# Optimization experiments

Hardware: AMD Instinct MI355X
Metric: run time of the kernel (lower is better)

The kernel has to match this reference:

```python
import jax, jax.numpy as jnp
import numpy as np

B, S, D_IN, D_OUT = 4, 4096, 256, 64


def setup_inputs() -> dict:
    key = jax.random.key(0)
    k1, k2, k3, k4, k5, k6 = jax.random.split(key, 6)
    return {
        "inputs_for_keys": jax.random.normal(k1, (B, S, D_IN), dtype=jnp.float32),
        "inputs_for_values": jax.random.normal(k2, (B, S, D_IN), dtype=jnp.float32),
        "inputs_for_queries": jax.random.normal(k3, (B, S, D_IN), dtype=jnp.float32),
        "wq": jax.random.normal(k4, (D_IN, D_OUT), dtype=jnp.float32) * 0.05,
        "wk": jax.random.normal(k5, (D_IN, D_OUT), dtype=jnp.float32) * 0.05,
        "wv": jax.random.normal(k6, (D_IN, D_OUT), dtype=jnp.float32) * 0.05,
    }


def reference(inputs_for_keys, inputs_for_values, inputs_for_queries, wq, wk, wv):
    # Linear projections: [B,S,D_IN] x [D_IN,D_OUT] -> [B,S,D_OUT]
    K = jnp.einsum("bsd,de->bse", inputs_for_keys, wk)
    V = jnp.einsum("bsd,de->bse", inputs_for_values, wv)
    Q = jnp.einsum("bsd,de->bse", inputs_for_queries, wq)
    d = K.shape[2]
    # Scaled dot-product scores: [B, S_q, S_k]
    scores = jnp.einsum("bqe,bke->bqk", Q, K) / jnp.sqrt(jnp.float32(d))
    # Causal mask: -inf where key index j > query index i (strict upper triangle)
    q_idx = jnp.arange(Q.shape[1])[:, None]
    k_idx = jnp.arange(K.shape[1])[None, :]
    mask = jnp.where(k_idx > q_idx, -jnp.inf, 0.0).astype(scores.dtype)
    scores = scores + mask[None, :, :]
    weights = jax.nn.softmax(scores, axis=-1)
    return jnp.einsum("bqk,bke->bqe", weights, V)
```

## Files before the change

kernel.cpp:

```cpp
#include <hip/hip_runtime.h>

#define S_LEN 4096
#define D_IN 256
#define D_OUT 64
#define BATCH 4
#define BQ 128
#define NQT (S_LEN / BQ)

typedef short bf16x8 __attribute__((ext_vector_type(8)));
typedef float f32x4 __attribute__((ext_vector_type(4)));

union L16 { int4 i; bf16x8 s; ushort u[8]; };
union U8  { uint2 d; ushort u[4]; };

#define SWZ(row, chunk) (((row) << 7) + ((((chunk) ^ ((row) & 7))) << 4))

#define QSCALE 0.1803368801111137f

__device__ inline ushort f2bf(float x) {
    unsigned u = __builtin_bit_cast(unsigned, x);
    u += 0x7FFFu + ((u >> 16) & 1u);
    return (ushort)(u >> 16);
}
__device__ inline ushort f2bf_t(float x) {
    return (ushort)(__builtin_bit_cast(unsigned, x) >> 16);
}
__device__ inline float bf2f(ushort h) {
    return __builtin_bit_cast(float, (unsigned)h << 16);
}

__global__ __launch_bounds__(256) void wsplit_kernel(
    const float* __restrict__ wq, const float* __restrict__ wk, const float* __restrict__ wv,
    ushort* __restrict__ Wt)
{
    const float* W = (blockIdx.y == 0) ? wq : (blockIdx.y == 1) ? wk : wv;
    __shared__ float Ws[64][68];
    const int t  = threadIdx.x;
    const int k0 = blockIdx.x * 64;
#pragma unroll
    for (int i = 0; i < 4; ++i) {
        int idx = t + i * 256;
        int r = idx >> 4, c4 = (idx & 15) * 4;
        *reinterpret_cast<float4*>(&Ws[r][c4]) =
            *reinterpret_cast<const float4*>(&W[(size_t)(k0 + r) * 64 + c4]);
    }
    __syncthreads();
    const int n = t >> 2, kc = t & 3;
    ushort h[16];
#pragma unroll
    for (int i = 0; i < 16; ++i) h[i] = f2bf(Ws[kc * 16 + i][n]);
    ushort* dst = Wt + ((size_t)blockIdx.y * 64 + n) * 256 + k0 + kc * 16;
    *reinterpret_cast<int4*>(dst)     = *reinterpret_cast<int4*>(h);
    *reinterpret_cast<int4*>(dst + 8) = *reinterpret_cast<int4*>(h + 8);
}

__global__ __launch_bounds__(256) void proj_kernel(
    const float* __restrict__ Xq, const float* __restrict__ Xk, const float* __restrict__ Xv,
    const ushort* __restrict__ Wt,
    ushort* __restrict__ Qb, ushort* __restrict__ Kb, ushort* __restrict__ Vtb)
{
    const float* X = (blockIdx.y == 0) ? Xq : (blockIdx.y == 1) ? Xk : Xv;
    const ushort* Wtp = Wt + (size_t)blockIdx.y * 64 * 256;

    __shared__ __align__(16) ushort Ob[64][64];

    const int t    = threadIdx.x;
    const int lane = t & 63;
    const int w    = t >> 6;
    const int n    = lane & 15;
    const int g    = lane >> 4;
    const int row0 = blockIdx.x * 64;

    const float* xrow = X + (size_t)(row0 + 16 * w + n) * D_IN;

    f32x4 acc[4];
    const f32x4 zero4 = {0.f, 0.f, 0.f, 0.f};
#pragma unroll
    for (int nt = 0; nt < 4; ++nt) acc[nt] = zero4;

#pragma unroll
    for (int kt = 0; kt < 8; ++kt) {
        const float4 c0 = *reinterpret_cast<const float4*>(xrow + kt * 32 + 8 * g);
        const float4 c1 = *reinterpret_cast<const float4*>(xrow + kt * 32 + 8 * g + 4);
        L16 wb[4];
#pragma unroll
        for (int nt = 0; nt < 4; ++nt)
            wb[nt].i = *reinterpret_cast<const int4*>(
                &Wtp[(size_t)(16 * nt + n) * 256 + kt * 32 + 8 * g]);

        const float xv[8] = {c0.x, c0.y, c0.z, c0.w, c1.x, c1.y, c1.z, c1.w};
        L16 xh, xl;
#pragma unroll
        for (int i = 0; i < 8; ++i) {
            ushort h = f2bf(xv[i]);
            xh.u[i] = h;
            xl.u[i] = f2bf(xv[i] - bf2f(h));
        }
#pragma unroll
        for (int nt = 0; nt < 4; ++nt) {
            acc[nt] = __builtin_amdgcn_mfma_f32_16x16x32_bf16(xh.s, wb[nt].s, acc[nt], 0, 0, 0);
            acc[nt] = __builtin_amdgcn_mfma_f32_16x16x32_bf16(xl.s, wb[nt].s, acc[nt], 0, 0, 0);
        }
    }

    const bool isV = (blockIdx.y == 2);
    const float oscale = (blockIdx.y == 0) ? QSCALE : 1.0f;
#pragma unroll
    for (int j = 0; j < 4; ++j) {
#pragma unroll
        for (int nt = 0; nt < 4; ++nt) {
            ushort h = f2bf(acc[nt][j] * oscale);
            int r = 16 * w + 4 * g + j;
            int c = 16 * nt + n;
            if (isV) Ob[c][r] = h; else Ob[r][c] = h;
        }
    }
    __syncthreads();
    const int b  = row0 >> 12;
    const int s0 = row0 & 4095;
#pragma unroll
    for (int i = 0; i < 2; ++i) {
        int idx = t + i * 256;
        int r = idx >> 3, c8 = (idx & 7) * 8;
        int4 v = *reinterpret_cast<const int4*>(&Ob[r][c8]);
        if (blockIdx.y == 0)
            *reinterpret_cast<int4*>(&Qb[(size_t)(row0 + r) * 64 + c8]) = v;
        else if (blockIdx.y == 1)
            *reinterpret_cast<int4*>(&Kb[(size_t)(row0 + r) * 64 + c8]) = v;
        else
            *reinterpret_cast<int4*>(&Vtb[((size_t)b * 64 + r) * S_LEN + s0 + c8]) = v;
    }
}

__global__ __launch_bounds__(256) void attn_kernel(
    const ushort* __restrict__ Q, const ushort* __restrict__ K,
    const ushort* __restrict__ Vt, float* __restrict__ O,
    ushort* __restrict__ Opart, float* __restrict__ Mpart, float* __restrict__ Lpart,
    int chunk_keys, int NCH, int lr4q, int Llive)
{
    __shared__ __align__(16) ushort Ks[2][64 * 64];
    __shared__ __align__(16) ushort Vs[2][64 * 64];
    __shared__ __align__(16) ushort Ps[4 * 16 * 64];

    const int Rq = 1 << lr4q;

    const int b = blockIdx.x & 3;
    const int f = blockIdx.x >> 2;
    int c = 0;
    while (NQT * (c + 1) - ((Rq * (c + 1) * c) >> 1) <= f) ++c;
    const int off  = NQT * c - ((Rq * c * (c - 1)) >> 1);
    const int qt   = (NQT - 1) - (f - off);
    const int ch   = c;
    const int q0   = qt * BQ;
    const int c0   = ch * chunk_keys;
    const int nchq = (qt >> lr4q) + 1;

    const int t    = threadIdx.x;
    const int lane = t & 63;
    const int w    = t >> 6;
    const int n    = lane & 15;
    const int g    = lane >> 4;

    const int kend = (c0 + chunk_keys < q0 + BQ) ? c0 + chunk_keys : q0 + BQ;
    const int kt0  = c0 >> 6;
    const int kt1  = (kend + 63) >> 6;

    const ushort* Qp = Q  + (size_t)b * S_LEN * 64;
    const ushort* Kp = K  + (size_t)b * S_LEN * 64;
    const ushort* Vp = Vt + (size_t)b * 64 * S_LEN;

    char* PsB = (char*)Ps + w * 2048;

    const int wqmin = q0 + 32 * w;
    const int wqmax = wqmin + 31;

    L16 aq[2][2];
#pragma unroll
    for (int h = 0; h < 2; ++h) {
        const size_t qr = (size_t)(wqmin + 16 * h + n) * 64;
        aq[h][0].i = *reinterpret_cast<const int4*>(&Qp[qr + 8 * g]);
        aq[h][1].i = *reinterpret_cast<const int4*>(&Qp[qr + 32 + 8 * g]);
    }

    L16 ones;
    ones.i = make_int4(0x3F803F80, 0x3F803F80, 0x3F803F80, 0x3F803F80);

    f32x4 oacc[2][4];
    const f32x4 zero4 = {0.f, 0.f, 0.f, 0.f};
#pragma unroll
    for (int h = 0; h < 2; ++h)
#pragma unroll
        for (int nt = 0; nt < 4; ++nt) oacc[h][nt] = zero4;
    float mreg[2] = {-1e30f, -1e30f}, lreg[2] = {0.f, 0.f};

    const int srow = t >> 3, sc = t & 7;

    auto load_tile = [&](int4 (&kr)[2], int4 (&vr)[2], int kt_) {
        const int kk0 = kt_ << 6;
#pragma unroll
        for (int i = 0; i < 2; ++i) {
            int row = srow + i * 32;
            kr[i] = *reinterpret_cast<const int4*>(&Kp[(size_t)(kk0 + row) * 64 + sc * 8]);
            vr[i] = *reinterpret_cast<const int4*>(&Vp[(size_t)row * S_LEN + kk0 + sc * 8]);
        }
    };
    auto store_tile = [&](int buf, const int4 (&kr)[2], const int4 (&vr)[2]) {
        char* kb = (char*)Ks + buf * 8192;
        char* vb = (char*)Vs + buf * 8192;
#pragma unroll
        for (int i = 0; i < 2; ++i) {
            int row = srow + i * 32;
            *reinterpret_cast<int4*>(kb + SWZ(row, sc)) = kr[i];
            *reinterpret_cast<int4*>(vb + SWZ(row, sc)) = vr[i];
        }
    };

    int4 kv[2], vv[2];
    load_tile(kv, vv, kt0);
    store_tile(0, kv, vv);
    if (kt0 + 1 < kt1) load_tile(kv, vv, kt0 + 1);
    __syncthreads();

    int cur = 0;
    for (int kt = kt0; kt < kt1; ++kt) {
        const int k0 = kt << 6;
        if (kt + 1 < kt1) {
            store_tile(cur ^ 1, kv, vv);
            if (kt + 2 < kt1) load_tile(kv, vv, kt + 2);
        }

        if (k0 <= wqmax) {
            char* KsB = (char*)Ks + cur * 8192;
            char* VsB = (char*)Vs + cur * 8192;

            f32x4 cS[2][4];
            __builtin_amdgcn_s_setprio(1);
#pragma unroll
            for (int t4 = 0; t4 < 4; ++t4) {
                L16 k0f, k1f;
                k0f.i = *reinterpret_cast<const int4*>(KsB + SWZ(16 * t4 + n, g));
                k1f.i = *reinterpret_cast<const int4*>(KsB + SWZ(16 * t4 + n, 4 + g));
#pragma unroll
                for (int h = 0; h < 2; ++h) {
                    f32x4 z = zero4;
                    z          = __builtin_amdgcn_mfma_f32_16x16x32_bf16(k0f.s, aq[h][0].s, z, 0, 0, 0);
                    cS[h][t4]  = __builtin_amdgcn_mfma_f32_16x16x32_bf16(k1f.s, aq[h][1].s, z, 0, 0, 0);
                }
            }
            __builtin_amdgcn_s_setprio(0);

#pragma unroll
            for (int h = 0; h < 2; ++h) {
                const int qrow = wqmin + 16 * h + n;
                float sc4[4][4];
#pragma unroll
                for (int t4 = 0; t4 < 4; ++t4)
#pragma unroll
                    for (int j = 0; j < 4; ++j) sc4[t4][j] = cS[h][t4][j];
                if (k0 + 63 > qrow) {
                    const int kb = k0 + 4 * g;
#pragma unroll
                    for (int t4 = 0; t4 < 4; ++t4)
#pragma unroll
                        for (int j = 0; j < 4; ++j)
                            if (kb + 16 * t4 + j > qrow) sc4[t4][j] = -1e30f;
                }

                float m0 = fmaxf(fmaxf(sc4[0][0], sc4[0][1]), fmaxf(sc4[0][2], sc4[0][3]));
                float m1 = fmaxf(fmaxf(sc4[1][0], sc4[1][1]), fmaxf(sc4[1][2], sc4[1][3]));
                float m2 = fmaxf(fmaxf(sc4[2][0], sc4[2][1]), fmaxf(sc4[2][2], sc4[2][3]));
                float m3 = fmaxf(fmaxf(sc4[3][0], sc4[3][1]), fmaxf(sc4[3][2], sc4[3][3]));
                const float lmax = fmaxf(fmaxf(m0, m1), fmaxf(m2, m3));

                if (__any(lmax > mreg[h] + 8.f)) {
                    float mx = lmax;
                    mx = fmaxf(mx, __shfl_xor(mx, 16, 64));
                    mx = fmaxf(mx, __shfl_xor(mx, 32, 64));
                    const float mnew  = fmaxf(mreg[h], mx);
                    const float alpha = exp2f(mreg[h] - mnew);
                    mreg[h] = mnew;
                    lreg[h] *= alpha;
#pragma unroll
                    for (int nt = 0; nt < 4; ++nt)
#pragma unroll
                        for (int j = 0; j < 4; ++j) oacc[h][nt][j] *= alpha;
                }

#pragma unroll
                for (int t4 = 0; t4 < 4; ++t4) {
                    U8 pw;
#pragma unroll
                    for (int j = 0; j < 4; ++j)
                        pw.u[j] = f2bf_t(exp2f(sc4[t4][j] - mreg[h]));
                    *reinterpret_cast<uint2*>(PsB + SWZ(n, 2 * t4 + (g >> 1)) + 8 * (g & 1)) = pw.d;
                }

                asm volatile("s_waitcnt lgkmcnt(0)" ::: "memory");
                L16 pa0, pa1;
                pa0.i = *reinterpret_cast<const int4*>(PsB + SWZ(n, g));
                pa1.i = *reinterpret_cast<const int4*>(PsB + SWZ(n, 4 + g));
                f32x4 ls = zero4;
                ls = __builtin_amdgcn_mfma_f32_16x16x32_bf16(ones.s, pa0.s, ls, 0, 0, 0);
                ls = __builtin_amdgcn_mfma_f32_16x16x32_bf16(ones.s, pa1.s, ls, 0, 0, 0);
                __builtin_amdgcn_s_setprio(1);
#pragma unroll
                for (int nt = 0; nt < 4; ++nt) {
                    L16 bv0, bv1;
                    bv0.i = *reinterpret_cast<const int4*>(VsB + SWZ(16 * nt + n, g));
                    bv1.i = *reinterpret_cast<const int4*>(VsB + SWZ(16 * nt + n, 4 + g));
                    oacc[h][nt] = __builtin_amdgcn_mfma_f32_16x16x32_bf16(bv0.s, pa0.s, oacc[h][nt], 0, 0, 0);
                    oacc[h][nt] = __builtin_amdgcn_mfma_f32_16x16x32_bf16(bv1.s, pa1.s, oacc[h][nt], 0, 0, 0);
                }
                __builtin_amdgcn_s_setprio(0);
                lreg[h] += ls[0];
            }
        }
        __syncthreads();
        cur ^= 1;
    }

    if (nchq == 1) {
#pragma unroll
        for (int h = 0; h < 2; ++h) {
            const float inv = 1.f / lreg[h];
            float* orow = O + ((size_t)b * S_LEN + wqmin + 16 * h + n) * 64;
#pragma unroll
            for (int nt = 0; nt < 4; ++nt)
#pragma unroll
                for (int j = 0; j < 4; ++j)
                    orow[16 * nt + 4 * g + j] = oacc[h][nt][j] * inv;
        }
    } else {
        const size_t slot = (size_t)((qt << 2) | b) * NCH + ch;
#pragma unroll
        for (int h = 0; h < 2; ++h) {
#pragma unroll
            for (int nt = 0; nt < 4; ++nt) {
                U8 pw;
#pragma unroll
                for (int j = 0; j < 4; ++j) pw.u[j] = f2bf(oacc[h][nt][j]);
                *reinterpret_cast<uint2*>(PsB + SWZ(n, 2 * nt + (g >> 1)) + 8 * (g & 1)) = pw.d;
            }
            asm volatile("s_waitcnt lgkmcnt(0)" ::: "memory");
            ushort* dst = Opart + slot * (BQ * 64) + w * 2048 + h * 1024;
#pragma unroll
            for (int i = 0; i < 2; ++i) {
                int ii = i * 64 + lane;
                *reinterpret_cast<int4*>(dst + ii * 8) =
                    *reinterpret_cast<const int4*>((const char*)PsB + ii * 16);
            }
        }
        if (g == 0) {
#pragma unroll
            for (int h = 0; h < 2; ++h) {
                Mpart[slot * BQ + 32 * w + 16 * h + n] = mreg[h];
                Lpart[slot * BQ + 32 * w + 16 * h + n] = lreg[h];
            }
        }
    }
}

__global__ __launch_bounds__(256) void reduce_kernel(
    const ushort* __restrict__ Opart, const float* __restrict__ Mpart,
    const float* __restrict__ Lpart, float* __restrict__ O,
    int NCH, int chunk_keys)
{
    const int bx  = blockIdx.x >> 2;
    const int seg = blockIdx.x & 3;
    const int b   = bx & 3;
    const int qt  = bx >> 2;
    const int q0  = qt * BQ;
    const int nch = (q0 + BQ + chunk_keys - 1) / chunk_keys;
    if (nch <= 1) return;

    const int t    = threadIdx.x;
    const int row  = seg * 32 + (t >> 3);
    const int c8   = t & 7;
    const int wv   = row >> 5, rl = row & 31;
    const int cswz = (c8 ^ (rl & 7)) << 4;

    const size_t mbase = (size_t)bx * NCH * BQ + row;
    float mmax = -1e30f;
    for (int ch = 0; ch < nch; ++ch)
        mmax = fmaxf(mmax, Mpart[mbase + (size_t)ch * BQ]);

    float ltot = 0.f;
    float acc[8];
#pragma unroll
    for (int i = 0; i < 8; ++i) acc[i] = 0.f;

    for (int ch = 0; ch < nch; ++ch) {
        const float wgt = exp2f(Mpart[mbase + (size_t)ch * BQ] - mmax);
        ltot += wgt * Lpart[mbase + (size_t)ch * BQ];
        const char* ob = (const char*)(Opart + ((size_t)bx * NCH + ch) * (BQ * 64))
                         + wv * 4096 + rl * 128 + cswz;
        L16 v;
        v.i = *reinterpret_cast<const int4*>(ob);
#pragma unroll
        for (int i = 0; i < 8; ++i) acc[i] += wgt * bf2f(v.u[i]);
    }
    const float inv = 1.f / ltot;
    float* dst = O + ((size_t)b * S_LEN + q0 + row) * 64 + c8 * 8;
#pragma unroll
    for (int i = 0; i < 2; ++i) {
        float4 o = make_float4(acc[4 * i] * inv, acc[4 * i + 1] * inv,
                               acc[4 * i + 2] * inv, acc[4 * i + 3] * inv);
        *reinterpret_cast<float4*>(dst + i * 4) = o;
    }
}

extern "C" void kernel_launch(void* const* d_in, const int* in_sizes, int n_in,
                              void* d_out, int out_size, void* d_ws, size_t ws_size,
                              hipStream_t stream) {
    const float* Xk = (const float*)d_in[0];
    const float* Xv = (const float*)d_in[1];
    const float* Xq = (const float*)d_in[2];
    const float* wq = (const float*)d_in[3];
    const float* wk = (const float*)d_in[4];
    const float* wv = (const float*)d_in[5];
    float* out = (float*)d_out;

    const size_t NEL = (size_t)BATCH * S_LEN * D_OUT;
    ushort* Qb  = (ushort*)d_ws;
    ushort* Kb  = Qb + NEL;
    ushort* Vtb = Kb + NEL;
    const size_t base_bytes = 3 * NEL * sizeof(ushort);
    const size_t per_nch    = (size_t)BATCH * NQT *
                              (BQ * 64 * sizeof(ushort) + 2 * BQ * sizeof(float));

    int NCH = 1;
    if      (ws_size >= base_bytes + 16 * per_nch) NCH = 16;
    else if (ws_size >= base_bytes +  8 * per_nch) NCH = 8;
    else if (ws_size >= base_bytes +  4 * per_nch) NCH = 4;
    else if (ws_size >= base_bytes +  2 * per_nch) NCH = 2;
    const int chunk_keys = S_LEN / NCH;
    const int Rq = chunk_keys / BQ;
    int lr4q = 0; while ((1 << lr4q) < Rq) ++lr4q;
    const int Llive = NCH * NQT - Rq * ((NCH * (NCH - 1)) >> 1);

    ushort* Wt    = (ushort*)((char*)d_ws + base_bytes);
    ushort* Opart = (ushort*)((char*)d_ws + base_bytes);
    float*  Mpart = (float*)((char*)d_ws + base_bytes +
                             (size_t)BATCH * NQT * NCH * BQ * 64 * sizeof(ushort));
    float*  Lpart = Mpart + (size_t)BATCH * NQT * NCH * BQ;

    wsplit_kernel<<<dim3(4, 3), 256, 0, stream>>>(wq, wk, wv, Wt);

    proj_kernel<<<dim3(BATCH * S_LEN / 64, 3), 256, 0, stream>>>(
        Xq, Xk, Xv, Wt, Qb, Kb, Vtb);

    attn_kernel<<<4 * Llive, 256, 0, stream>>>(Qb, Kb, Vtb, out, Opart, Mpart, Lpart,
                                               chunk_keys, NCH, lr4q, Llive);
    if (NCH > 1)
        reduce_kernel<<<BATCH * NQT * 4, 256, 0, stream>>>(Opart, Mpart, Lpart, out,
                                                           NCH, chunk_keys);
}
```

Baseline: 81.26 us.

## Load K/V MFMA fragments directly from global memory instead of staging through LDS

Removes the double-buffered shared-memory staging of K and V tiles, along with the per-tile __syncthreads. Each wave now reads its MFMA operand fragments straight from global memory (relying on L1/L2 caching) and runs its own loop bound, clamped to its causal limit. This removes the LDS stores, the barriers and the cross-wave coupling, and lets waves skip tiles entirely past their diagonal. In exchange it loses the explicit prefetch and software pipelining, and each of the four waves reads the same K/V data separately through the cache, with global-load latency now exposed right before the MFMAs.

```diff
diff --git a/kernel.cpp b/kernel.cpp
--- a/kernel.cpp
+++ b/kernel.cpp
@@ -138,8 +138,6 @@
     ushort* __restrict__ Opart, float* __restrict__ Mpart, float* __restrict__ Lpart,
     int chunk_keys, int NCH, int lr4q, int Llive)
 {
-    __shared__ __align__(16) ushort Ks[2][64 * 64];
-    __shared__ __align__(16) ushort Vs[2][64 * 64];
     __shared__ __align__(16) ushort Ps[4 * 16 * 64];
 
     const int Rq = 1 << lr4q;
@@ -173,6 +171,7 @@
 
     const int wqmin = q0 + 32 * w;
     const int wqmax = wqmin + 31;
+    const int kt1w  = (kt1 < ((wqmax >> 6) + 1)) ? kt1 : ((wqmax >> 6) + 1);
 
     L16 aq[2][2];
 #pragma unroll
@@ -193,130 +192,92 @@
         for (int nt = 0; nt < 4; ++nt) oacc[h][nt] = zero4;
     float mreg[2] = {-1e30f, -1e30f}, lreg[2] = {0.f, 0.f};
 
-    const int srow = t >> 3, sc = t & 7;
-
-    auto load_tile = [&](int4 (&kr)[2], int4 (&vr)[2], int kt_) {
-        const int kk0 = kt_ << 6;
-#pragma unroll
-        for (int i = 0; i < 2; ++i) {
-            int row = srow + i * 32;
-            kr[i] = *reinterpret_cast<const int4*>(&Kp[(size_t)(kk0 + row) * 64 + sc * 8]);
-            vr[i] = *reinterpret_cast<const int4*>(&Vp[(size_t)row * S_LEN + kk0 + sc * 8]);
-        }
-    };
-    auto store_tile = [&](int buf, const int4 (&kr)[2], const int4 (&vr)[2]) {
-        char* kb = (char*)Ks + buf * 8192;
-        char* vb = (char*)Vs + buf * 8192;
-#pragma unroll
-        for (int i = 0; i < 2; ++i) {
-            int row = srow + i * 32;
-            *reinterpret_cast<int4*>(kb + SWZ(row, sc)) = kr[i];
-            *reinterpret_cast<int4*>(vb + SWZ(row, sc)) = vr[i];
-        }
-    };
-
-    int4 kv[2], vv[2];
-    load_tile(kv, vv, kt0);
-    store_tile(0, kv, vv);
-    if (kt0 + 1 < kt1) load_tile(kv, vv, kt0 + 1);
-    __syncthreads();
-
-    int cur = 0;
-    for (int kt = kt0; kt < kt1; ++kt) {
+    for (int kt = kt0; kt < kt1w; ++kt) {
         const int k0 = kt << 6;
-        if (kt + 1 < kt1) {
-            store_tile(cur ^ 1, kv, vv);
-            if (kt + 2 < kt1) load_tile(kv, vv, kt + 2);
-        }
-
-        if (k0 <= wqmax) {
-            char* KsB = (char*)Ks + cur * 8192;
-            char* VsB = (char*)Vs + cur * 8192;
-
-            f32x4 cS[2][4];
+        const ushort* Kt = Kp + (size_t)k0 * 64;
+        const ushort* Vc = Vp + k0;
+
+        f32x4 cS[2][4];
+#pragma unroll
+        for (int t4 = 0; t4 < 4; ++t4) {
+            L16 k0f, k1f;
+            k0f.i = *reinterpret_cast<const int4*>(&Kt[(size_t)(16 * t4 + n) * 64 + 8 * g]);
+            k1f.i = *reinterpret_cast<const int4*>(&Kt[(size_t)(16 * t4 + n) * 64 + 32 + 8 * g]);
             __builtin_amdgcn_s_setprio(1);
 #pragma unroll
+            for (int h = 0; h < 2; ++h) {
+                f32x4 z = zero4;
+                z          = __builtin_amdgcn_mfma_f32_16x16x32_bf16(k0f.s, aq[h][0].s, z, 0, 0, 0);
+                cS[h][t4]  = __builtin_amdgcn_mfma_f32_16x16x32_bf16(k1f.s, aq[h][1].s, z, 0, 0, 0);
+            }
+            __builtin_amdgcn_s_setprio(0);
+        }
+
+#pragma unroll
+        for (int h = 0; h < 2; ++h) {
+            const int qrow = wqmin + 16 * h + n;
+            float sc4[4][4];
+#pragma unroll
+            for (int t4 = 0; t4 < 4; ++t4)
+#pragma unroll
+                for (int j = 0; j < 4; ++j) sc4[t4][j] = cS[h][t4][j];
+            if (k0 + 63 > qrow) {
+                const int kb = k0 + 4 * g;
+#pragma unroll
+                for (int t4 = 0; t4 < 4; ++t4)
+#pragma unroll
+                    for (int j = 0; j < 4; ++j)
+                        if (kb + 16 * t4 + j > qrow) sc4[t4][j] = -1e30f;
+            }
+
+            float m0 = fmaxf(fmaxf(sc4[0][0], sc4[0][1]), fmaxf(sc4[0][2], sc4[0][3]));
+            float m1 = fmaxf(fmaxf(sc4[1][0], sc4[1][1]), fmaxf(sc4[1][2], sc4[1][3]));
+            float m2 = fmaxf(fmaxf(sc4[2][0], sc4[2][1]), fmaxf(sc4[2][2], sc4[2][3]));
+            float m3 = fmaxf(fmaxf(sc4[3][0], sc4[3][1]), fmaxf(sc4[3][2], sc4[3][3]));
+            const float lmax = fmaxf(fmaxf(m0, m1), fmaxf(m2, m3));
+
+            if (__any(lmax > mreg[h] + 8.f)) {
+                float mx = lmax;
+                mx = fmaxf(mx, __shfl_xor(mx, 16, 64));
+                mx = fmaxf(mx, __shfl_xor(mx, 32, 64));
+                const float mnew  = fmaxf(mreg[h], mx);
+                const float alpha = exp2f(mreg[h] - mnew);
+                mreg[h] = mnew;
+                lreg[h] *= alpha;
+#pragma unroll
+                for (int nt = 0; nt < 4; ++nt)
+#pragma unroll
+                    for (int j = 0; j < 4; ++j) oacc[h][nt][j] *= alpha;
+            }
+
+#pragma unroll
             for (int t4 = 0; t4 < 4; ++t4) {
-                L16 k0f, k1f;
-                k0f.i = *reinterpret_cast<const int4*>(KsB + SWZ(16 * t4 + n, g));
-                k1f.i = *reinterpret_cast<const int4*>(KsB + SWZ(16 * t4 + n, 4 + g));
-#pragma unroll
-                for (int h = 0; h < 2; ++h) {
-                    f32x4 z = zero4;
-                    z          = __builtin_amdgcn_mfma_f32_16x16x32_bf16(k0f.s, aq[h][0].s, z, 0, 0, 0);
-                    cS[h][t4]  = __builtin_amdgcn_mfma_f32_16x16x32_bf16(k1f.s, aq[h][1].s, z, 0, 0, 0);
-                }
-            }
-            __builtin_amdgcn_s_setprio(0);
-
-#pragma unroll
-            for (int h = 0; h < 2; ++h) {
-                const int qrow = wqmin + 16 * h + n;
-                float sc4[4][4];
-#pragma unroll
-                for (int t4 = 0; t4 < 4; ++t4)
-#pragma unroll
-                    for (int j = 0; j < 4; ++j) sc4[t4][j] = cS[h][t4][j];
-                if (k0 + 63 > qrow) {
-                    const int kb = k0 + 4 * g;
-#pragma unroll
-                    for (int t4 = 0; t4 < 4; ++t4)
-#pragma unroll
-                        for (int j = 0; j < 4; ++j)
-                            if (kb + 16 * t4 + j > qrow) sc4[t4][j] = -1e30f;
-                }
-
-                float m0 = fmaxf(fmaxf(sc4[0][0], sc4[0][1]), fmaxf(sc4[0][2], sc4[0][3]));
-                float m1 = fmaxf(fmaxf(sc4[1][0], sc4[1][1]), fmaxf(sc4[1][2], sc4[1][3]));
-                float m2 = fmaxf(fmaxf(sc4[2][0], sc4[2][1]), fmaxf(sc4[2][2], sc4[2][3]));
-                float m3 = fmaxf(fmaxf(sc4[3][0], sc4[3][1]), fmaxf(sc4[3][2], sc4[3][3]));
-                const float lmax = fmaxf(fmaxf(m0, m1), fmaxf(m2, m3));
-
-                if (__any(lmax > mreg[h] + 8.f)) {
-                    float mx = lmax;
-                    mx = fmaxf(mx, __shfl_xor(mx, 16, 64));
-                    mx = fmaxf(mx, __shfl_xor(mx, 32, 64));
-                    const float mnew  = fmaxf(mreg[h], mx);
-                    const float alpha = exp2f(mreg[h] - mnew);
-                    mreg[h] = mnew;
-                    lreg[h] *= alpha;
-#pragma unroll
-                    for (int nt = 0; nt < 4; ++nt)
-#pragma unroll
-                        for (int j = 0; j < 4; ++j) oacc[h][nt][j] *= alpha;
-                }
-
-#pragma unroll
-                for (int t4 = 0; t4 < 4; ++t4) {
-                    U8 pw;
-#pragma unroll
-                    for (int j = 0; j < 4; ++j)
-                        pw.u[j] = f2bf_t(exp2f(sc4[t4][j] - mreg[h]));
-                    *reinterpret_cast<uint2*>(PsB + SWZ(n, 2 * t4 + (g >> 1)) + 8 * (g & 1)) = pw.d;
-                }
-
-                asm volatile("s_waitcnt lgkmcnt(0)" ::: "memory");
-                L16 pa0, pa1;
-                pa0.i = *reinterpret_cast<const int4*>(PsB + SWZ(n, g));
-                pa1.i = *reinterpret_cast<const int4*>(PsB + SWZ(n, 4 + g));
-                f32x4 ls = zero4;
-                ls = __builtin_amdgcn_mfma_f32_16x16x32_bf16(ones.s, pa0.s, ls, 0, 0, 0);
-                ls = __builtin_amdgcn_mfma_f32_16x16x32_bf16(ones.s, pa1.s, ls, 0, 0, 0);
+                U8 pw;
+#pragma unroll
+                for (int j = 0; j < 4; ++j)
+                    pw.u[j] = f2bf_t(exp2f(sc4[t4][j] - mreg[h]));
+                *reinterpret_cast<uint2*>(PsB + SWZ(n, 2 * t4 + (g >> 1)) + 8 * (g & 1)) = pw.d;
+            }
+
+            asm volatile("s_waitcnt lgkmcnt(0)" ::: "memory");
+            L16 pa0, pa1;
+            pa0.i = *reinterpret_cast<const int4*>(PsB + SWZ(n, g));
+            pa1.i = *reinterpret_cast<const int4*>(PsB + SWZ(n, 4 + g));
+            f32x4 ls = zero4;
+            ls = __builtin_amdgcn_mfma_f32_16x16x32_bf16(ones.s, pa0.s, ls, 0, 0, 0);
+            ls = __builtin_amdgcn_mfma_f32_16x16x32_bf16(ones.s, pa1.s, ls, 0, 0, 0);
+#pragma unroll
+            for (int nt = 0; nt < 4; ++nt) {
+                L16 bv0, bv1;
+                bv0.i = *reinterpret_cast<const int4*>(&Vc[(size_t)(16 * nt + n) * S_LEN + 8 * g]);
+                bv1.i = *reinterpret_cast<const int4*>(&Vc[(size_t)(16 * nt + n) * S_LEN + 32 + 8 * g]);
                 __builtin_amdgcn_s_setprio(1);
-#pragma unroll
-                for (int nt = 0; nt < 4; ++nt) {
-                    L16 bv0, bv1;
-                    bv0.i = *reinterpret_cast<const int4*>(VsB + SWZ(16 * nt + n, g));
-                    bv1.i = *reinterpret_cast<const int4*>(VsB + SWZ(16 * nt + n, 4 + g));
-                    oacc[h][nt] = __builtin_amdgcn_mfma_f32_16x16x32_bf16(bv0.s, pa0.s, oacc[h][nt], 0, 0, 0);
-                    oacc[h][nt] = __builtin_amdgcn_mfma_f32_16x16x32_bf16(bv1.s, pa1.s, oacc[h][nt], 0, 0, 0);
-                }
+                oacc[h][nt] = __builtin_amdgcn_mfma_f32_16x16x32_bf16(bv0.s, pa0.s, oacc[h][nt], 0, 0, 0);
+                oacc[h][nt] = __builtin_amdgcn_mfma_f32_16x16x32_bf16(bv1.s, pa1.s, oacc[h][nt], 0, 0, 0);
                 __builtin_amdgcn_s_setprio(0);
-                lreg[h] += ls[0];
-            }
-        }
-        __syncthreads();
-        cur ^= 1;
+            }
+            lreg[h] += ls[0];
+        }
     }
 
     if (nchq == 1) {
```

Result: slower. 107.2 us (+31.9%).
